# Kernel tuning notes

Hardware: AMD Instinct MI355X
Metric: run time of the kernel (lower is better)

The kernel has to match this reference:

```python
import jax, jax.numpy as jnp
import numpy as np

IN, H, T = 1024, 2048, 2048

def setup_inputs() -> dict:
    key = jax.random.key(0)
    ks = jax.random.split(key, 10)
    x = jax.random.normal(ks[0], (1, T, IN), dtype=jnp.float32)
    # strictly increasing timestamps
    time = jnp.cumsum(jax.random.uniform(ks[1], (T,), dtype=jnp.float32))
    # xavier-ish scaled weights, uniform(0,1) biases as in init_weights
    W_ih = jax.random.normal(ks[2], (4 * H, IN), dtype=jnp.float32) * (1.0 / np.sqrt(IN))
    W_hh = jax.random.normal(ks[3], (4 * H, H), dtype=jnp.float32) * (1.0 / np.sqrt(H))
    b_ih = jax.random.uniform(ks[4], (4 * H,), dtype=jnp.float32)
    b_hh = jax.random.uniform(ks[5], (4 * H,), dtype=jnp.float32)
    decay_w = jax.random.normal(ks[6], (H,), dtype=jnp.float32)
    decay_b = jax.random.uniform(ks[7], (H,), dtype=jnp.float32)
    h0 = jax.random.normal(ks[8], (1, H), dtype=jnp.float32) * 0.1
    c0 = jax.random.normal(ks[9], (1, H), dtype=jnp.float32) * 0.1
    return {"x": x, "time": time, "W_ih": W_ih, "W_hh": W_hh, "b_ih": b_ih,
            "b_hh": b_hh, "decay_w": decay_w, "decay_b": decay_b, "h0": h0, "c0": c0}


def reference(x, time, W_ih, W_hh, b_ih, b_hh, decay_w, decay_b, h0, c0):
    Tn = x.shape[1]
    Hn = h0.shape[1]
    # dt[i] = time[i] - time[i-1], dt[0] = 0
    dt = jnp.concatenate([jnp.zeros((1,), x.dtype), time[1:] - time[:-1]])
    # step i (i>0) decays h with gamma(dt[i-1]); step 0 uses gamma = 1
    dt_prev = jnp.concatenate([jnp.zeros((1,), x.dtype), dt[:-1]])  # [T]
    gamma = jnp.exp(-jax.nn.relu(dt_prev[:, None] * decay_w[None, :] + decay_b[None, :]))  # [T,H]
    gamma = jnp.where((jnp.arange(Tn) > 0)[:, None], gamma, jnp.ones((), x.dtype))
    # precompute input contribution for all steps: [T, 4H]
    xg = x[0] @ W_ih.T + b_ih + b_hh

    def step(carry, inp):
        h, c = carry  # [H], [H]
        xg_t, gamma_t = inp
        h = h * gamma_t
        gates = xg_t + h @ W_hh.T  # [4H]
        i_, f_, g_, o_ = jnp.split(gates, 4)
        i_ = jax.nn.sigmoid(i_)
        f_ = jax.nn.sigmoid(f_)
        g_ = jnp.tanh(g_)
        o_ = jax.nn.sigmoid(o_)
        c = f_ * c + i_ * g_
        h = o_ * jnp.tanh(c)
        return (h, c), h

    (h_f, c_f), hs = jax.lax.scan(step, (h0[0], c0[0]), (xg, gamma))  # hs: [T,H]
    # dot-product attention pooling against final hidden state
    attn = hs @ h_f  # [T]
    w = jax.nn.softmax(attn)
    context = w @ hs  # [H]
    return context[None, :]  # [1, H]
```

## Files before the change

### kernel.cpp

```cpp
#include <hip/hip_runtime.h>
#include <hip/hip_bf16.h>

#define H 2048
#define T 2048
#define INPUT 1024
#define FOURH 8192
#define NBLK 256
#define RING 512

typedef __attribute__((ext_vector_type(8))) short bf16x8;
typedef __attribute__((ext_vector_type(4))) float f32x4_t;

__device__ __forceinline__ unsigned short f2bf(float f) {
  union { float f; unsigned u; } v; v.f = f;
  unsigned r = v.u + 0x7FFFu + ((v.u >> 16) & 1u);
  return (unsigned short)(r >> 16);
}

__global__ void prep_kernel(const float* __restrict__ x, const float* __restrict__ W_ih,
                            const float* __restrict__ time_, short* __restrict__ xb,
                            short* __restrict__ wb, float* __restrict__ dtp,
                            unsigned* __restrict__ flags) {
  size_t i = (size_t)blockIdx.x * blockDim.x + threadIdx.x;
  size_t stride = (size_t)gridDim.x * blockDim.x;
  if (i < (size_t)T * INPUT) xb[i] = (short)f2bf(x[i]);
  for (size_t j = i; j < (size_t)FOURH * INPUT; j += stride) wb[j] = (short)f2bf(W_ih[j]);
  if (i < T) dtp[i] = (i >= 2) ? (time_[i - 1] - time_[i - 2]) : 0.0f;
  if (i < NBLK) flags[i] = 0u;
}

__global__ void __launch_bounds__(256)
gemm_xg(const short* __restrict__ A, const short* __restrict__ B,
        const float* __restrict__ b_ih, const float* __restrict__ b_hh,
        float* __restrict__ xg) {
  int wave = threadIdx.x >> 6;
  int lane = threadIdx.x & 63;
  int bid = blockIdx.x;
  int m0 = (bid & 127) << 4;
  int n0 = ((bid >> 7) << 6) + (wave << 4);
  int r16 = lane & 15, q = lane >> 4;
  const short* ap = A + (size_t)(m0 + r16) * INPUT + q * 8;
  const short* bp = B + (size_t)(n0 + r16) * INPUT + q * 8;
  f32x4_t acc = {0.f, 0.f, 0.f, 0.f};
#pragma unroll 4
  for (int k = 0; k < INPUT; k += 32) {
    bf16x8 av = *(const bf16x8*)(ap + k);
    bf16x8 bv = *(const bf16x8*)(bp + k);
    acc = __builtin_amdgcn_mfma_f32_16x16x32_bf16(av, bv, acc, 0, 0, 0);
  }
  int n = n0 + r16;
  float bias = b_ih[n] + b_hh[n];
#pragma unroll
  for (int r = 0; r < 4; ++r) {
    int m = m0 + q * 4 + r;
    xg[(size_t)m * FOURH + n] = acc[r] + bias;
  }
}

__device__ __forceinline__ void epoch_bar(unsigned* flags, unsigned e) {
  __syncthreads();
  if (threadIdx.x == 0)
    __hip_atomic_store(&flags[blockIdx.x], e, __ATOMIC_RELEASE, __HIP_MEMORY_SCOPE_AGENT);
  if (threadIdx.x < NBLK) {
    while (__hip_atomic_load(&flags[threadIdx.x], __ATOMIC_RELAXED,
                             __HIP_MEMORY_SCOPE_AGENT) < e) {
    }
  }
  __builtin_amdgcn_fence(__ATOMIC_ACQUIRE, "agent");
  __syncthreads();
}

__global__ void __launch_bounds__(512, 2)
lstm_rec(const float* __restrict__ xg, const float* __restrict__ W_hh,
         const float* __restrict__ decay_w, const float* __restrict__ decay_b,
         const float* __restrict__ h0, const float* __restrict__ c0,
         const float* __restrict__ dtp, float* __restrict__ hs,
         unsigned long long* ring, unsigned* flags) {
  const int wave = threadIdx.x >> 6;
  const int lane = threadIdx.x & 63;
  const int u = (blockIdx.x << 3) + wave;
  __shared__ __align__(16) float lh[H];

  float wreg[4][32];
#pragma unroll
  for (int g = 0; g < 4; ++g) {
    const float* wr = W_hh + (size_t)(g * H + u) * H + (lane << 2);
#pragma unroll
    for (int p = 0; p < 8; ++p)
      *(f32x4_t*)&wreg[g][p << 2] = *(const f32x4_t*)(wr + (p << 8));
  }
  const float dw = decay_w[u], db = decay_b[u];
  float c = c0[u];
  if (lane == 0) {
    union { float f; unsigned u; } hv; hv.f = h0[u];
    __hip_atomic_store(&ring[u], (1ull << 32) | hv.u, __ATOMIC_RELAXED,
                       __HIP_MEMORY_SCOPE_AGENT);
  }

  for (int t = 0; t < T; ++t) {
    if ((t & 255) == 0 && t) epoch_bar(flags, (unsigned)(t >> 8));

    float xi = 0.f, xf = 0.f, xgv = 0.f, xo = 0.f, gam = 0.f;
    if (lane == 0) {
      const float* xr = xg + (size_t)t * FOURH;
      xi = xr[u]; xf = xr[H + u]; xgv = xr[2 * H + u]; xo = xr[3 * H + u];
      if (t + 1 < T) gam = __expf(-fmaxf(0.f, dtp[t + 1] * dw + db));
    }

    const unsigned want = (unsigned)t + 1u;
    unsigned long long* sp =
        ring + (((size_t)(t & (RING - 1)) << 11) | (unsigned)((wave << 8) + lane));
    unsigned long long w0, w1, w2, w3;
    for (;;) {
      w0 = __hip_atomic_load(sp,       __ATOMIC_RELAXED, __HIP_MEMORY_SCOPE_AGENT);
      w1 = __hip_atomic_load(sp + 64,  __ATOMIC_RELAXED, __HIP_MEMORY_SCOPE_AGENT);
      w2 = __hip_atomic_load(sp + 128, __ATOMIC_RELAXED, __HIP_MEMORY_SCOPE_AGENT);
      w3 = __hip_atomic_load(sp + 192, __ATOMIC_RELAXED, __HIP_MEMORY_SCOPE_AGENT);
      int bad = ((unsigned)(w0 >> 32) != want) | ((unsigned)(w1 >> 32) != want) |
                ((unsigned)(w2 >> 32) != want) | ((unsigned)(w3 >> 32) != want);
      if (!__any(bad)) break;
    }
    {
      float* lw = lh + (wave << 8) + lane;
      union { unsigned u; float f; } v;
      v.u = (unsigned)w0; lw[0]   = v.f;
      v.u = (unsigned)w1; lw[64]  = v.f;
      v.u = (unsigned)w2; lw[128] = v.f;
      v.u = (unsigned)w3; lw[192] = v.f;
    }
    __syncthreads();

    float a0 = 0.f, a1 = 0.f, a2 = 0.f, a3 = 0.f;
#pragma unroll
    for (int p = 0; p < 8; ++p) {
      f32x4_t h4 = *(const f32x4_t*)(lh + (p << 8) + (lane << 2));
#pragma unroll
      for (int e = 0; e < 4; ++e) {
        float h = h4[e];
        a0 += wreg[0][(p << 2) + e] * h;
        a1 += wreg[1][(p << 2) + e] * h;
        a2 += wreg[2][(p << 2) + e] * h;
        a3 += wreg[3][(p << 2) + e] * h;
      }
    }
#pragma unroll
    for (int s = 32; s >= 1; s >>= 1) {
      a0 += __shfl_xor(a0, s);
      a1 += __shfl_xor(a1, s);
      a2 += __shfl_xor(a2, s);
      a3 += __shfl_xor(a3, s);
    }
    if (lane == 0) {
      float iv = a0 + xi;
      float fv = a1 + xf;
      float gv = a2 + xgv;
      float ov = a3 + xo;
      iv = 1.f / (1.f + __expf(-iv));
      fv = 1.f / (1.f + __expf(-fv));
      gv = tanhf(gv);
      ov = 1.f / (1.f + __expf(-ov));
      c = fv * c + iv * gv;
      float h = ov * tanhf(c);
      if (t + 1 < T) {
        union { float f; unsigned u; } hv; hv.f = h * gam;
        size_t slot = (size_t)((t + 1) & (RING - 1)) << 11;
        __hip_atomic_store(&ring[slot | (unsigned)u],
                           (((unsigned long long)(t + 2)) << 32) | hv.u,
                           __ATOMIC_RELAXED, __HIP_MEMORY_SCOPE_AGENT);
      }
      hs[(size_t)t * H + u] = h;
    }
    __syncthreads();
  }
}

__global__ void attn_k(const float* __restrict__ hs, float* __restrict__ attn) {
  int t = blockIdx.x;
  const float* row = hs + (size_t)t * H;
  const float* hf = hs + (size_t)(T - 1) * H;
  float s = 0.f;
  for (int i = threadIdx.x; i < H; i += 256) s += row[i] * hf[i];
#pragma unroll
  for (int o = 32; o; o >>= 1) s += __shfl_down(s, o);
  __shared__ float wsum[4];
  if ((threadIdx.x & 63) == 0) wsum[threadIdx.x >> 6] = s;
  __syncthreads();
  if (threadIdx.x == 0) attn[t] = wsum[0] + wsum[1] + wsum[2] + wsum[3];
}

__global__ void softmax_k(float* __restrict__ a) {
  int tid = threadIdx.x;
  __shared__ float red[16];
  __shared__ float bcast;
  float m = -1e30f;
  for (int i = tid; i < T; i += 1024) m = fmaxf(m, a[i]);
#pragma unroll
  for (int o = 32; o; o >>= 1) m = fmaxf(m, __shfl_xor(m, o));
  if ((tid & 63) == 0) red[tid >> 6] = m;
  __syncthreads();
  if (tid == 0) {
    float mm = red[0];
    for (int i = 1; i < 16; ++i) mm = fmaxf(mm, red[i]);
    bcast = mm;
  }
  __syncthreads();
  float M = bcast, s = 0.f;
  for (int i = tid; i < T; i += 1024) { float e = __expf(a[i] - M); a[i] = e; s += e; }
#pragma unroll
  for (int o = 32; o; o >>= 1) s += __shfl_xor(s, o);
  if ((tid & 63) == 0) red[tid >> 6] = s;
  __syncthreads();
  if (tid == 0) {
    float ss = 0.f;
    for (int i = 0; i < 16; ++i) ss += red[i];
    bcast = 1.f / ss;
  }
  __syncthreads();
  float inv = bcast;
  for (int i = tid; i < T; i += 1024) a[i] *= inv;
}

__global__ void ctx_k(const float* __restrict__ hs, const float* __restrict__ w,
                      float* __restrict__ out) {
  int h = (blockIdx.x << 8) + threadIdx.x;
  int t0 = blockIdx.y << 6;
  float acc = 0.f;
  for (int t = t0; t < t0 + 64; ++t) acc += w[t] * hs[(size_t)t * H + h];
  atomicAdd(&out[h], acc);
}

extern "C" void kernel_launch(void* const* d_in, const int* in_sizes, int n_in,
                              void* d_out, int out_size, void* d_ws, size_t ws_size,
                              hipStream_t stream) {
  const float* x       = (const float*)d_in[0];
  const float* time_   = (const float*)d_in[1];
  const float* W_ih    = (const float*)d_in[2];
  const float* W_hh    = (const float*)d_in[3];
  const float* b_ih    = (const float*)d_in[4];
  const float* b_hh    = (const float*)d_in[5];
  const float* decay_w = (const float*)d_in[6];
  const float* decay_b = (const float*)d_in[7];
  const float* h0      = (const float*)d_in[8];
  const float* c0      = (const float*)d_in[9];

  char* ws = (char*)d_ws;
  float*    xg   = (float*)ws;
  float*    hs   = (float*)(ws + (64u << 20));
  short*    xb   = (short*)(ws + (80u << 20));
  short*    wb   = (short*)(ws + (84u << 20));
  unsigned long long* ring = (unsigned long long*)(ws + (100u << 20));
  float*    dtp  = (float*)(ws + (108u << 20));
  float*    attn = dtp + T;
  unsigned* flags = (unsigned*)(attn + T);

  prep_kernel<<<8192, 256, 0, stream>>>(x, W_ih, time_, xb, wb, dtp, flags);

  gemm_xg<<<16384, 256, 0, stream>>>(xb, wb, b_ih, b_hh, xg);

  {
    void* args[] = {&xg, (void*)&W_hh, (void*)&decay_w, (void*)&decay_b,
                    (void*)&h0, (void*)&c0, &dtp, &hs, &ring, &flags};
    (void)hipLaunchCooperativeKernel((void*)lstm_rec, dim3(NBLK), dim3(512), args, 0, stream);
  }

  attn_k<<<T, 256, 0, stream>>>(hs, attn);
  softmax_k<<<1, 1024, 0, stream>>>(attn);
  (void)hipMemsetAsync(d_out, 0, out_size * sizeof(float), stream);
  ctx_k<<<dim3(H / 256, T / 64), 256, 0, stream>>>(hs, attn, (float*)d_out);
}
```

Measured before the change: 6.466 ms.

## Replace per-step block barriers with per-wave LDS flags and double-buffered hidden state

```diff
diff --git a/kernel.cpp b/kernel.cpp
--- a/kernel.cpp
+++ b/kernel.cpp
@@ -15,6 +15,11 @@
   union { float f; unsigned u; } v; v.f = f;
   unsigned r = v.u + 0x7FFFu + ((v.u >> 16) & 1u);
   return (unsigned short)(r >> 16);
+}
+
+__device__ __forceinline__ float fast_tanh(float x) {
+  float e = __expf(fminf(-2.f * x, 80.f));
+  return (1.f - e) / (1.f + e);
 }
 
 __global__ void prep_kernel(const float* __restrict__ x, const float* __restrict__ W_ih,
@@ -79,68 +84,88 @@
   const int wave = threadIdx.x >> 6;
   const int lane = threadIdx.x & 63;
   const int u = (blockIdx.x << 3) + wave;
-  __shared__ __align__(16) float lh[H];
+  __shared__ __align__(16) float lh[2][H];
+  __shared__ unsigned lflag[8];
 
   float wreg[4][32];
 #pragma unroll
   for (int g = 0; g < 4; ++g) {
     const float* wr = W_hh + (size_t)(g * H + u) * H + (lane << 2);
 #pragma unroll
-    for (int p = 0; p < 8; ++p)
-      *(f32x4_t*)&wreg[g][p << 2] = *(const f32x4_t*)(wr + (p << 8));
+    for (int j = 0; j < 8; ++j) {
+      int p = (wave + j) & 7;
+      *(f32x4_t*)&wreg[g][j << 2] = *(const f32x4_t*)(wr + (p << 8));
+    }
   }
   const float dw = decay_w[u], db = decay_b[u];
   float c = c0[u];
+  if (threadIdx.x < 8) lflag[threadIdx.x] = 0u;
   if (lane == 0) {
     union { float f; unsigned u; } hv; hv.f = h0[u];
     __hip_atomic_store(&ring[u], (1ull << 32) | hv.u, __ATOMIC_RELAXED,
                        __HIP_MEMORY_SCOPE_AGENT);
   }
+  __syncthreads();
+
+#define POLL4(d0, d1, d2, d3)                                                          \
+  d0 = __hip_atomic_load(sp, __ATOMIC_RELAXED, __HIP_MEMORY_SCOPE_AGENT);              \
+  d1 = __hip_atomic_load(sp + 64, __ATOMIC_RELAXED, __HIP_MEMORY_SCOPE_AGENT);         \
+  d2 = __hip_atomic_load(sp + 128, __ATOMIC_RELAXED, __HIP_MEMORY_SCOPE_AGENT);        \
+  d3 = __hip_atomic_load(sp + 192, __ATOMIC_RELAXED, __HIP_MEMORY_SCOPE_AGENT);
 
   for (int t = 0; t < T; ++t) {
     if ((t & 255) == 0 && t) epoch_bar(flags, (unsigned)(t >> 8));
 
-    float xi = 0.f, xf = 0.f, xgv = 0.f, xo = 0.f, gam = 0.f;
-    if (lane == 0) {
-      const float* xr = xg + (size_t)t * FOURH;
-      xi = xr[u]; xf = xr[H + u]; xgv = xr[2 * H + u]; xo = xr[3 * H + u];
-      if (t + 1 < T) gam = __expf(-fmaxf(0.f, dtp[t + 1] * dw + db));
-    }
+    float xv = 0.f, gam = 0.f;
+    if (lane < 4) xv = xg[(size_t)t * FOURH + (size_t)lane * H + u];
+    if (lane == 0 && t + 1 < T) gam = __expf(-fmaxf(0.f, dtp[t + 1] * dw + db));
 
     const unsigned want = (unsigned)t + 1u;
     unsigned long long* sp =
         ring + (((size_t)(t & (RING - 1)) << 11) | (unsigned)((wave << 8) + lane));
-    unsigned long long w0, w1, w2, w3;
+    unsigned long long w0, w1, w2, w3, v0, v1, v2, v3;
+    POLL4(w0, w1, w2, w3)
     for (;;) {
-      w0 = __hip_atomic_load(sp,       __ATOMIC_RELAXED, __HIP_MEMORY_SCOPE_AGENT);
-      w1 = __hip_atomic_load(sp + 64,  __ATOMIC_RELAXED, __HIP_MEMORY_SCOPE_AGENT);
-      w2 = __hip_atomic_load(sp + 128, __ATOMIC_RELAXED, __HIP_MEMORY_SCOPE_AGENT);
-      w3 = __hip_atomic_load(sp + 192, __ATOMIC_RELAXED, __HIP_MEMORY_SCOPE_AGENT);
-      int bad = ((unsigned)(w0 >> 32) != want) | ((unsigned)(w1 >> 32) != want) |
-                ((unsigned)(w2 >> 32) != want) | ((unsigned)(w3 >> 32) != want);
-      if (!__any(bad)) break;
-    }
+      POLL4(v0, v1, v2, v3)
+      bool ok = ((unsigned)(w0 >> 32) == want) & ((unsigned)(w1 >> 32) == want) &
+                ((unsigned)(w2 >> 32) == want) & ((unsigned)(w3 >> 32) == want);
+      if (__all(ok)) break;
+      POLL4(w0, w1, w2, w3)
+      ok = ((unsigned)(v0 >> 32) == want) & ((unsigned)(v1 >> 32) == want) &
+           ((unsigned)(v2 >> 32) == want) & ((unsigned)(v3 >> 32) == want);
+      if (__all(ok)) { w0 = v0; w1 = v1; w2 = v2; w3 = v3; break; }
+    }
+
+    float* base = lh[t & 1];
     {
-      float* lw = lh + (wave << 8) + lane;
+      float* lw = base + (wave << 8) + lane;
       union { unsigned u; float f; } v;
       v.u = (unsigned)w0; lw[0]   = v.f;
       v.u = (unsigned)w1; lw[64]  = v.f;
       v.u = (unsigned)w2; lw[128] = v.f;
       v.u = (unsigned)w3; lw[192] = v.f;
     }
-    __syncthreads();
+    if (lane == 0)
+      __hip_atomic_store(&lflag[wave], want, __ATOMIC_RELEASE,
+                         __HIP_MEMORY_SCOPE_WORKGROUP);
 
     float a0 = 0.f, a1 = 0.f, a2 = 0.f, a3 = 0.f;
 #pragma unroll
-    for (int p = 0; p < 8; ++p) {
-      f32x4_t h4 = *(const f32x4_t*)(lh + (p << 8) + (lane << 2));
+    for (int j = 0; j < 8; ++j) {
+      int p = (wave + j) & 7;
+      if (j) {
+        while (__hip_atomic_load(&lflag[p], __ATOMIC_ACQUIRE,
+                                 __HIP_MEMORY_SCOPE_WORKGROUP) < want) {
+        }
+      }
+      f32x4_t h4 = *(const f32x4_t*)(base + (p << 8) + (lane << 2));
 #pragma unroll
       for (int e = 0; e < 4; ++e) {
         float h = h4[e];
-        a0 += wreg[0][(p << 2) + e] * h;
-        a1 += wreg[1][(p << 2) + e] * h;
-        a2 += wreg[2][(p << 2) + e] * h;
-        a3 += wreg[3][(p << 2) + e] * h;
+        a0 += wreg[0][(j << 2) + e] * h;
+        a1 += wreg[1][(j << 2) + e] * h;
+        a2 += wreg[2][(j << 2) + e] * h;
+        a3 += wreg[3][(j << 2) + e] * h;
       }
     }
 #pragma unroll
@@ -150,28 +175,29 @@
       a2 += __shfl_xor(a2, s);
       a3 += __shfl_xor(a3, s);
     }
-    if (lane == 0) {
-      float iv = a0 + xi;
-      float fv = a1 + xf;
-      float gv = a2 + xgv;
-      float ov = a3 + xo;
-      iv = 1.f / (1.f + __expf(-iv));
-      fv = 1.f / (1.f + __expf(-fv));
-      gv = tanhf(gv);
-      ov = 1.f / (1.f + __expf(-ov));
+
+    {
+      float pre = ((lane == 0) ? a0 : (lane == 1) ? a1 : (lane == 2) ? a2 : a3) + xv;
+      float ps = (lane == 2) ? 2.f * pre : pre;
+      float sg = 1.f / (1.f + __expf(-ps));
+      float act = (lane == 2) ? 2.f * sg - 1.f : sg;
+      float iv = __shfl(act, 0), fv = __shfl(act, 1), gv = __shfl(act, 2),
+            ov = __shfl(act, 3);
       c = fv * c + iv * gv;
-      float h = ov * tanhf(c);
-      if (t + 1 < T) {
-        union { float f; unsigned u; } hv; hv.f = h * gam;
-        size_t slot = (size_t)((t + 1) & (RING - 1)) << 11;
-        __hip_atomic_store(&ring[slot | (unsigned)u],
-                           (((unsigned long long)(t + 2)) << 32) | hv.u,
-                           __ATOMIC_RELAXED, __HIP_MEMORY_SCOPE_AGENT);
+      float h = ov * fast_tanh(c);
+      if (lane == 0) {
+        if (t + 1 < T) {
+          union { float f; unsigned u; } hv; hv.f = h * gam;
+          size_t slot = (size_t)((t + 1) & (RING - 1)) << 11;
+          __hip_atomic_store(&ring[slot | (unsigned)u],
+                             (((unsigned long long)(t + 2)) << 32) | hv.u,
+                             __ATOMIC_RELAXED, __HIP_MEMORY_SCOPE_AGENT);
+        }
+        hs[(size_t)t * H + u] = h;
       }
-      hs[(size_t)t * H + u] = h;
-    }
-    __syncthreads();
-  }
+    }
+  }
+#undef POLL4
 }
 
 __global__ void attn_k(const float* __restrict__ hs, float* __restrict__ attn) {
```

Measured after the change: 13.21 ms. 104% more time.
